# Performance work log

Measured on AMD Instinct MI355X. Metric: run time of the kernel, lower is better.

The kernel has to match this reference:

```python
import jax, jax.numpy as jnp
import numpy as np

D_MODEL = 512
NHEAD = 8
HEAD_DIM = D_MODEL // NHEAD  # 64, also rotary_dim
WIN_LO, WIN_HI = 127, 128    # attn_window: kv in [q-127, q+128]
BLOCK = 256                  # block size for banded attention (>= WIN_LO+1 and >= WIN_HI)


def setup_inputs() -> dict:
    key = jax.random.key(0)
    k1, k2, k3, k4 = jax.random.split(key, 4)
    N, T = 4, 2048
    x = jax.random.normal(k1, (N, T, D_MODEL), dtype=jnp.float32)
    Wqkv_w = jax.random.normal(k2, (3 * D_MODEL, D_MODEL), dtype=jnp.float32) * 0.02
    out_w = jax.random.normal(k3, (D_MODEL, D_MODEL), dtype=jnp.float32) * 0.02
    out_b = jax.random.normal(k4, (D_MODEL,), dtype=jnp.float32) * 0.02
    return {"x": x, "Wqkv_w": Wqkv_w, "out_w": out_w, "out_b": out_b}


def _rotate_half(u):
    u1, u2 = jnp.split(u, 2, axis=-1)
    return jnp.concatenate((-u2, u1), axis=-1)


def _apply_rope(q, k, T, dtype):
    # inv_freq: [HEAD_DIM/2]
    inv_freq = 1.0 / (10000.0 ** (jnp.arange(0, HEAD_DIM, 2, dtype=jnp.float32) / HEAD_DIM))
    pos = jnp.arange(T, dtype=dtype)
    freqs = pos[:, None] * inv_freq[None, :].astype(dtype)      # [T, D/2]
    emb = jnp.concatenate((freqs, freqs), axis=-1)              # [T, D]
    cos = jnp.cos(emb)[None, :, None, :]                        # [1,T,1,D]
    sin = jnp.sin(emb)[None, :, None, :]
    q = q * cos + _rotate_half(q) * sin
    k = k * cos + _rotate_half(k) * sin
    return q, k


def reference(x, Wqkv_w, out_w, out_b):
    N, T, dm = x.shape
    H, D, B = NHEAD, HEAD_DIM, BLOCK
    qkv = (x @ Wqkv_w.T).reshape(N, T, 3, H, D)
    q, k, v = qkv[:, :, 0], qkv[:, :, 1], qkv[:, :, 2]          # [N,T,H,D]
    q, k = _apply_rope(q, k, T, x.dtype)
    # [N,H,T,D]
    q = q.transpose(0, 2, 1, 3)
    k = k.transpose(0, 2, 1, 3)
    v = v.transpose(0, 2, 1, 3)

    nb = T // B
    qb = q.reshape(N, H, nb, B, D)
    kb = k.reshape(N, H, nb, B, D)
    vb = v.reshape(N, H, nb, B, D)
    # pad one block of zeros on each side so block g sees key blocks g-1,g,g+1
    pad = ((0, 0), (0, 0), (1, 1), (0, 0), (0, 0))
    kp = jnp.pad(kb, pad)
    vp = jnp.pad(vb, pad)
    # [N,H,nb,3B,D]
    kwin = jnp.concatenate([kp[:, :, i:i + nb] for i in range(3)], axis=3)
    vwin = jnp.concatenate([vp[:, :, i:i + nb] for i in range(3)], axis=3)

    scale = 1.0 / np.sqrt(D)
    scores = jnp.einsum('nhgqd,nhgkd->nhgqk', qb, kwin) * scale  # [N,H,nb,B,3B]

    qi = jnp.arange(B)
    kj = jnp.arange(3 * B)
    gidx = jnp.arange(nb)
    diff = kj[None, None, :] - B - qi[None, :, None]             # [1,B,3B] kv - q offset
    band = (diff >= -WIN_LO) & (diff <= WIN_HI)
    kv_global = gidx[:, None, None] * B + kj[None, None, :] - B  # [nb,1,3B]
    valid = (kv_global >= 0) & (kv_global < T)
    mask = band & valid                                          # [nb,B,3B]

    neg = jnp.asarray(-1e30, dtype=scores.dtype)
    scores = jnp.where(mask[None, None], scores, neg)
    probs = jax.nn.softmax(scores, axis=-1)
    attn = jnp.einsum('nhgqk,nhgkd->nhgqd', probs, vwin)         # [N,H,nb,B,D]
    attn = attn.reshape(N, H, T, D).transpose(0, 2, 1, 3).reshape(N, T, dm)
    return attn @ out_w.T + out_b
```

## Files before the change

kernel.cpp:

```cpp
#include <hip/hip_runtime.h>
#include <math.h>


typedef __attribute__((ext_vector_type(8))) __bf16 bf16x8;
typedef __attribute__((ext_vector_type(4))) float f32x4;

__device__ __forceinline__ unsigned short f2bf(float f) {
    unsigned int u = __float_as_uint(f);
    u += 0x7fffu + ((u >> 16) & 1u);
    return (unsigned short)(u >> 16);
}
__device__ __forceinline__ unsigned int packbf2(float a, float b) {
    unsigned int ua = __float_as_uint(a); ua += 0x7fffu + ((ua >> 16) & 1u);
    unsigned int ub = __float_as_uint(b); ub += 0x7fffu + ((ub >> 16) & 1u);
    return (ua >> 16) | (ub & 0xffff0000u);
}
__device__ __forceinline__ bf16x8 as_bf16x8(uint4 u) {
    union { uint4 u4; bf16x8 v; } c; c.u4 = u; return c.v;
}
__device__ __forceinline__ bf16x8 ld_frag(const unsigned short* p) {
    return as_bf16x8(*(const uint4*)p);
}

__device__ __forceinline__ void async16(void* lds, const void* g) {
    __builtin_amdgcn_global_load_lds(
        (const __attribute__((address_space(1))) void*)g,
        (__attribute__((address_space(3))) void*)lds,
        16, 0, 0);
}

__global__ __launch_bounds__(256) void cvt_all(
    const float* __restrict__ x, const float* __restrict__ w1,
    const float* __restrict__ w2,
    unsigned short* __restrict__ xb, unsigned short* __restrict__ w1b,
    unsigned short* __restrict__ w2b)
{
    const int n_x  = 8192 * 512 / 4;
    const int n_w1 = 1536 * 512 / 4;
    const int n_w2 = 512 * 512 / 4;
    int i = blockIdx.x * 256 + threadIdx.x;
    const float* in; unsigned short* out; int j;
    if (i < n_x)                    { in = x;  out = xb;  j = i; }
    else if (i < n_x + n_w1)        { in = w1; out = w1b; j = i - n_x; }
    else if (i < n_x + n_w1 + n_w2) { in = w2; out = w2b; j = i - n_x - n_w1; }
    else return;
    float4 v = *(const float4*)(in + 4 * (size_t)j);
    uint2 o;
    o.x = packbf2(v.x, v.y);
    o.y = packbf2(v.z, v.w);
    *(uint2*)(out + 4 * (size_t)j) = o;
}

__global__ __launch_bounds__(256, 5) void gemm_bt_mfma(
    const unsigned short* __restrict__ A, const unsigned short* __restrict__ B,
    const float* __restrict__ bias, void* __restrict__ Cout,
    int M, int O, int K, int write_bf16, int do_rope,
    unsigned short* __restrict__ vT)
{
    __shared__ __align__(16) unsigned short As[128 * 64];
    __shared__ __align__(16) unsigned short Bs[64 * 64];

    const int tid  = threadIdx.x;
    const int wave = tid >> 6;
    const int lane = tid & 63;
    const int l15  = lane & 15;
    const int lg   = lane >> 4;
    const int row0 = blockIdx.x * 128;
    const int col0 = blockIdx.y * 64;
    const int wr   = wave * 32;

    f32x4 acc[2][4] = {};

    const int srow = tid >> 3;
    const int skg  = ((tid & 7) * 8) ^ ((srow & 7) * 8);
    const int fx   = (l15 & 7) * 8;

    for (int k0 = 0; k0 < K; k0 += 64) {
        #pragma unroll
        for (int s = 0; s < 4; ++s)
            async16(&As[(size_t)(s * 256 + tid) * 8],
                    A + (size_t)(row0 + s * 32 + srow) * K + k0 + skg);
        #pragma unroll
        for (int s = 0; s < 2; ++s)
            async16(&Bs[(size_t)(s * 256 + tid) * 8],
                    B + (size_t)(col0 + s * 32 + srow) * K + k0 + skg);
        __syncthreads();

        #pragma unroll
        for (int kstep = 0; kstep < 2; ++kstep) {
            const int kq = (kstep * 32 + lg * 8) ^ fx;
            bf16x8 af[2], bfr[4];
            #pragma unroll
            for (int mt = 0; mt < 2; ++mt)
                af[mt] = ld_frag(&As[(wr + mt * 16 + l15) * 64 + kq]);
            #pragma unroll
            for (int nt = 0; nt < 4; ++nt)
                bfr[nt] = ld_frag(&Bs[(nt * 16 + l15) * 64 + kq]);
            #pragma unroll
            for (int mt = 0; mt < 2; ++mt)
                #pragma unroll
                for (int nt = 0; nt < 4; ++nt)
                    acc[mt][nt] = __builtin_amdgcn_mfma_f32_16x16x32_bf16(
                        af[mt], bfr[nt], acc[mt][nt], 0, 0, 0);
        }
        __syncthreads();
    }

    const int qrow = lg * 4;

    if (do_rope && col0 < 1024) {
        const float cfreq = 0.28782313662425574f;
        const float invf0 = __expf(-(float)l15 * cfreq);
        const float invf1 = __expf(-(float)(16 + l15) * cfreq);
        #pragma unroll
        for (int mt = 0; mt < 2; ++mt) {
            #pragma unroll
            for (int r = 0; r < 4; ++r) {
                const int t = (row0 + wr + mt * 16 + qrow + r) & 2047;
                #pragma unroll
                for (int p = 0; p < 2; ++p) {
                    float ang = (float)t * (p ? invf1 : invf0);
                    float s, c;
                    __sincosf(ang, &s, &c);
                    float a = acc[mt][p][r];
                    float b = acc[mt][p + 2][r];
                    acc[mt][p][r]     = a * c - b * s;
                    acc[mt][p + 2][r] = b * c + a * s;
                }
            }
        }
        if (col0 < 512) {
            #pragma unroll
            for (int mt = 0; mt < 2; ++mt)
                #pragma unroll
                for (int nt = 0; nt < 4; ++nt)
                    #pragma unroll
                    for (int r = 0; r < 4; ++r)
                        acc[mt][nt][r] *= 0.125f;
        }
    }

    if (do_rope && col0 >= 1024) {
        #pragma unroll
        for (int nt = 0; nt < 4; ++nt) {
            const int local = col0 - 1024 + nt * 16 + l15;
            const int hh = local >> 6;
            const int dd = local & 63;
            #pragma unroll
            for (int mt = 0; mt < 2; ++mt) {
                const int rowb = row0 + wr + mt * 16 + qrow;
                const int nn = rowb >> 11;
                const int tt = rowb & 2047;
                uint2 o;
                o.x = packbf2(acc[mt][nt][0], acc[mt][nt][1]);
                o.y = packbf2(acc[mt][nt][2], acc[mt][nt][3]);
                *(uint2*)(vT + ((size_t)(nn * 8 + hh) * 64 + dd) * 2048 + tt) = o;
            }
        }
        return;
    }

    #pragma unroll
    for (int nt = 0; nt < 4; ++nt) {
        const int col = col0 + nt * 16 + l15;
        const float bv = bias ? bias[col] : 0.f;
        #pragma unroll
        for (int mt = 0; mt < 2; ++mt) {
            const int rowb = row0 + wr + mt * 16 + qrow;
            if (write_bf16) {
                unsigned short* C = (unsigned short*)Cout;
                #pragma unroll
                for (int r = 0; r < 4; ++r)
                    C[(size_t)(rowb + r) * O + col] = f2bf(acc[mt][nt][r] + bv);
            } else {
                float* C = (float*)Cout;
                #pragma unroll
                for (int r = 0; r < 4; ++r)
                    C[(size_t)(rowb + r) * O + col] = acc[mt][nt][r] + bv;
            }
        }
    }
}

__global__ __launch_bounds__(256) void attn_mfma_kernel(
    const unsigned short* __restrict__ qkv,
    const unsigned short* __restrict__ vT,
    unsigned short* __restrict__ attnout)
{
    __shared__ __align__(16) unsigned short Kt[64 * 72];
    __shared__ __align__(16) unsigned short Vt[64 * 72];
    __shared__ __align__(16) unsigned short Ps[4][16 * 72];

    const int qt = blockIdx.x;
    const int h  = blockIdx.y;
    const int n  = blockIdx.z;
    const int t0 = qt * 64;
    const int tid  = threadIdx.x;
    const int wave = tid >> 6;
    const int lane = tid & 63;
    const int l15  = lane & 15;
    const int lg   = lane >> 4;
    const int qrow = lg * 4;

    const size_t base = (size_t)n * 2048 * 1536 + (size_t)h * 64;
    const unsigned short* vTh = vT + (size_t)(n * 8 + h) * 64 * 2048;

    bf16x8 qfrag[2];
    {
        const unsigned short* qp = qkv + base + (size_t)(t0 + wave * 16 + l15) * 1536;
        qfrag[0] = ld_frag(qp + lg * 8);
        qfrag[1] = ld_frag(qp + 32 + lg * 8);
    }

    const int skey = tid >> 2;
    const int sd0  = (tid & 3) * 16;

    const int qq = wave * 16 + l15;
    float m_v = -1e30f, l_v = 0.f;
    f32x4 acc_o[4] = {};

    for (int dt = -2; dt <= 2; ++dt) {
        const int kt = qt + dt;
        if (kt < 0 || kt > 31) continue;
        const int s0 = kt * 64;

        {
            const unsigned short* kp = qkv + base + 512 + (size_t)(s0 + skey) * 1536 + sd0;
            *(uint4*)&Kt[skey * 72 + sd0]     = *(const uint4*)kp;
            *(uint4*)&Kt[skey * 72 + sd0 + 8] = *(const uint4*)(kp + 8);

            const unsigned short* vp = vTh + (size_t)skey * 2048 + s0 + sd0;
            *(uint4*)&Vt[skey * 72 + sd0]     = *(const uint4*)vp;
            *(uint4*)&Vt[skey * 72 + sd0 + 8] = *(const uint4*)(vp + 8);
        }
        __syncthreads();

        f32x4 acc_s[4] = {};
        #pragma unroll
        for (int kstep = 0; kstep < 2; ++kstep) {
            #pragma unroll
            for (int nt = 0; nt < 4; ++nt) {
                if ((dt == -2 && nt < wave) || (dt == 2 && nt > wave)) continue;
                bf16x8 kf = ld_frag(&Kt[(nt * 16 + l15) * 72 + kstep * 32 + lg * 8]);
                acc_s[nt] = __builtin_amdgcn_mfma_f32_16x16x32_bf16(
                    kf, qfrag[kstep], acc_s[nt], 0, 0, 0);
            }
        }

        float p[4][4];
        float tm = -1e30f;
        #pragma unroll
        for (int nt = 0; nt < 4; ++nt) {
            #pragma unroll
            for (int r = 0; r < 4; ++r) {
                const int diff = dt * 64 + nt * 16 + qrow + r - qq;
                const bool ok = (diff >= -127) && (diff <= 128);
                const float v = ok ? acc_s[nt][r] : -1e30f;
                p[nt][r] = v;
                tm = fmaxf(tm, v);
            }
        }
        tm = fmaxf(tm, __shfl_xor(tm, 16, 64));
        tm = fmaxf(tm, __shfl_xor(tm, 32, 64));
        const float m_new = fmaxf(m_v, tm);
        const float alpha = __expf(m_v - m_new);
        float psum = 0.f;
        #pragma unroll
        for (int nt = 0; nt < 4; ++nt) {
            #pragma unroll
            for (int r = 0; r < 4; ++r) {
                const float e = __expf(p[nt][r] - m_new);
                p[nt][r] = e;
                psum += e;
            }
        }
        psum += __shfl_xor(psum, 16, 64);
        psum += __shfl_xor(psum, 32, 64);
        l_v = l_v * alpha + psum;
        m_v = m_new;

        #pragma unroll
        for (int r = 0; r < 4; ++r) {
            const float a_r = __shfl(alpha, (lane & 48) + qrow + r, 64);
            #pragma unroll
            for (int nt = 0; nt < 4; ++nt) acc_o[nt][r] *= a_r;
        }

        #pragma unroll
        for (int nt = 0; nt < 4; ++nt) {
            uint2 o;
            o.x = packbf2(p[nt][0], p[nt][1]);
            o.y = packbf2(p[nt][2], p[nt][3]);
            *(uint2*)&Ps[wave][l15 * 72 + nt * 16 + qrow] = o;
        }

        __syncthreads();

        bf16x8 pfrag[2];
        pfrag[0] = ld_frag(&Ps[wave][l15 * 72 + lg * 8]);
        pfrag[1] = ld_frag(&Ps[wave][l15 * 72 + 32 + lg * 8]);

        #pragma unroll
        for (int kstep = 0; kstep < 2; ++kstep) {
            #pragma unroll
            for (int nt = 0; nt < 4; ++nt) {
                bf16x8 vf = ld_frag(&Vt[(nt * 16 + l15) * 72 + kstep * 32 + lg * 8]);
                acc_o[nt] = __builtin_amdgcn_mfma_f32_16x16x32_bf16(
                    pfrag[kstep], vf, acc_o[nt], 0, 0, 0);
            }
        }
        __syncthreads();
    }

    const float linv = 1.0f / l_v;
    float inv_l[4];
    #pragma unroll
    for (int r = 0; r < 4; ++r)
        inv_l[r] = __shfl(linv, (lane & 48) + qrow + r, 64);

    #pragma unroll
    for (int r = 0; r < 4; ++r) {
        const int tq = t0 + wave * 16 + qrow + r;
        unsigned short* op = attnout + (size_t)(n * 2048 + tq) * 512 + h * 64;
        #pragma unroll
        for (int nt = 0; nt < 4; ++nt)
            op[nt * 16 + l15] = f2bf(acc_o[nt][r] * inv_l[r]);
    }
}

extern "C" void kernel_launch(void* const* d_in, const int* in_sizes, int n_in,
                              void* d_out, int out_size, void* d_ws, size_t ws_size,
                              hipStream_t stream)
{
    (void)in_sizes; (void)n_in; (void)out_size; (void)ws_size;

    const float* x     = (const float*)d_in[0];
    const float* Wqkv  = (const float*)d_in[1];
    const float* out_w = (const float*)d_in[2];
    const float* out_b = (const float*)d_in[3];
    float* out = (float*)d_out;

    unsigned short* qkvb  = (unsigned short*)d_ws;
    unsigned short* attnb = qkvb + (size_t)8192 * 1536;
    unsigned short* xb    = attnb + (size_t)8192 * 512;
    unsigned short* wqkvb = xb + (size_t)8192 * 512;
    unsigned short* outwb = wqkvb + (size_t)1536 * 512;
    unsigned short* vTb   = outwb + (size_t)512 * 512;

    cvt_all<<<5120, 256, 0, stream>>>(x, Wqkv, out_w, xb, wqkvb, outwb);

    gemm_bt_mfma<<<dim3(64, 24), 256, 0, stream>>>(xb, wqkvb, nullptr, qkvb,
                                                   8192, 1536, 512, 1, 1, vTb);
    attn_mfma_kernel<<<dim3(32, 8, 4), 256, 0, stream>>>(qkvb, vTb, attnb);
    gemm_bt_mfma<<<dim3(64, 8), 256, 0, stream>>>(attnb, outwb, out_b, out,
                                                  8192, 512, 512, 0, 0, nullptr);
}
```

Baseline: 128.1 us.

## Double-buffer GEMM LDS tiles with async prefetch of next K slice

The bf16 MFMA GEMM now splits LDS into two K=32 buffers and issues async global-to-LDS loads for the next K slice before computing on the current one. Partial waits (vmcnt) plus raw barriers replace the full load-then-sync pattern. The aim is to overlap global memory latency with MFMA work. The cost is halving the K depth per iteration, which doubles the barrier count, and relying on a correct vmcnt count for the async loads.

After: 131.7 us. +2.8%, slower.

```diff
diff --git a/kernel.cpp b/kernel.cpp
--- a/kernel.cpp
+++ b/kernel.cpp
@@ -57,8 +57,8 @@
     int M, int O, int K, int write_bf16, int do_rope,
     unsigned short* __restrict__ vT)
 {
-    __shared__ __align__(16) unsigned short As[128 * 64];
-    __shared__ __align__(16) unsigned short Bs[64 * 64];
+    __shared__ __align__(16) unsigned short As[2][128 * 32];
+    __shared__ __align__(16) unsigned short Bs[2][64 * 32];
 
     const int tid  = threadIdx.x;
     const int wave = tid >> 6;
@@ -71,39 +71,58 @@
 
     f32x4 acc[2][4] = {};
 
-    const int srow = tid >> 3;
-    const int skg  = ((tid & 7) * 8) ^ ((srow & 7) * 8);
-    const int fx   = (l15 & 7) * 8;
-
-    for (int k0 = 0; k0 < K; k0 += 64) {
-        #pragma unroll
-        for (int s = 0; s < 4; ++s)
-            async16(&As[(size_t)(s * 256 + tid) * 8],
-                    A + (size_t)(row0 + s * 32 + srow) * K + k0 + skg);
+    const int sr2 = tid >> 2;
+    const int skg = ((tid & 3) * 8) ^ ((sr2 & 3) * 8);
+    const int fx3 = (l15 & 3) * 8;
+
+    const int NT = K >> 5;
+
+    {
         #pragma unroll
         for (int s = 0; s < 2; ++s)
-            async16(&Bs[(size_t)(s * 256 + tid) * 8],
-                    B + (size_t)(col0 + s * 32 + srow) * K + k0 + skg);
-        __syncthreads();
-
-        #pragma unroll
-        for (int kstep = 0; kstep < 2; ++kstep) {
-            const int kq = (kstep * 32 + lg * 8) ^ fx;
-            bf16x8 af[2], bfr[4];
-            #pragma unroll
-            for (int mt = 0; mt < 2; ++mt)
-                af[mt] = ld_frag(&As[(wr + mt * 16 + l15) * 64 + kq]);
+            async16(&As[0][(size_t)(s * 256 + tid) * 8],
+                    A + (size_t)(row0 + s * 64 + sr2) * K + skg);
+        async16(&Bs[0][(size_t)tid * 8],
+                B + (size_t)(col0 + sr2) * K + skg);
+    }
+    asm volatile("s_waitcnt vmcnt(0)" ::: "memory");
+    __builtin_amdgcn_sched_barrier(0);
+    __builtin_amdgcn_s_barrier();
+
+    for (int t = 0; t < NT; ++t) {
+        const int h = t & 1;
+        if (t + 1 < NT) {
+            const int h1 = h ^ 1;
+            const int kg = (t + 1) * 32 + skg;
+            #pragma unroll
+            for (int s = 0; s < 2; ++s)
+                async16(&As[h1][(size_t)(s * 256 + tid) * 8],
+                        A + (size_t)(row0 + s * 64 + sr2) * K + kg);
+            async16(&Bs[h1][(size_t)tid * 8],
+                    B + (size_t)(col0 + sr2) * K + kg);
+            asm volatile("s_waitcnt vmcnt(3)" ::: "memory");
+        } else {
+            asm volatile("s_waitcnt vmcnt(0)" ::: "memory");
+        }
+        __builtin_amdgcn_sched_barrier(0);
+        __builtin_amdgcn_s_barrier();
+
+        const int kq = (lg * 8) ^ fx3;
+        bf16x8 af[2], bfr[4];
+        #pragma unroll
+        for (int mt = 0; mt < 2; ++mt)
+            af[mt] = ld_frag(&As[h][(wr + mt * 16 + l15) * 32 + kq]);
+        #pragma unroll
+        for (int nt = 0; nt < 4; ++nt)
+            bfr[nt] = ld_frag(&Bs[h][(nt * 16 + l15) * 32 + kq]);
+        #pragma unroll
+        for (int mt = 0; mt < 2; ++mt)
             #pragma unroll
             for (int nt = 0; nt < 4; ++nt)
-                bfr[nt] = ld_frag(&Bs[(nt * 16 + l15) * 64 + kq]);
-            #pragma unroll
-            for (int mt = 0; mt < 2; ++mt)
-                #pragma unroll
-                for (int nt = 0; nt < 4; ++nt)
-                    acc[mt][nt] = __builtin_amdgcn_mfma_f32_16x16x32_bf16(
-                        af[mt], bfr[nt], acc[mt][nt], 0, 0, 0);
-        }
-        __syncthreads();
+                acc[mt][nt] = __builtin_amdgcn_mfma_f32_16x16x32_bf16(
+                    af[mt], bfr[nt], acc[mt][nt], 0, 0, 0);
+
+        __builtin_amdgcn_s_barrier();
     }
 
     const int qrow = lg * 4;
```
